# Kernel optimization log

Hardware: AMD Instinct MI355X
Metric: run time of the kernel (lower is better)

The kernel has to match this reference:

```python
import jax, jax.numpy as jnp
import numpy as np

DIM = 512; NHEAD = 8; DHEAD = 64; INNER = NHEAD * DHEAD
CTX = 1024; NOCT = int(np.ceil(np.log2(CTX))) + 1  # 11
B = 8; SEQ = 256; MEM = 768


def positional_encoding(ctx, num_oct):
    # matches Attention.positional_encoding on coords=arange(ctx).view(ctx,1),
    # start_octave = 1 - num_oct
    coords = jnp.arange(ctx, dtype=jnp.float32)[:, None, None]        # (ctx,1,1)
    octaves = jnp.arange(1 - num_oct, 1, dtype=jnp.float32)           # (num_oct,)
    mult = (2.0 ** octaves) * np.pi
    scaled = (coords * mult).reshape(ctx, num_oct)                    # (ctx, num_oct)
    return jnp.concatenate([jnp.sin(scaled), jnp.cos(scaled)], axis=-1)  # (ctx, 2*num_oct)


def get_shifts(mem, seq, ctx):
    coords = jnp.arange(mem + seq - 1, -1, -1) - (seq - 1)            # (mem+seq,)
    shifts = coords[None, :] + jnp.arange(seq)[:, None]               # (seq, mem+seq)
    oob = (shifts < 0) | (shifts > ctx - 1)
    bias = jnp.where(oob, -jnp.inf, 0.0).astype(jnp.float32)
    return jnp.clip(shifts, 0, ctx - 1), bias


def setup_inputs() -> dict:
    key = jax.random.key(0)
    ks = jax.random.split(key, 8)
    s = 0.02
    return {
        "x": jax.random.normal(ks[0], (B, SEQ, DIM), jnp.float32),
        "memory": jax.random.normal(ks[1], (B, MEM, DIM), jnp.float32),
        "W_qkv": jax.random.normal(ks[2], (DIM, 3 * INNER), jnp.float32) * s,
        "W_rel": jax.random.normal(ks[3], (2 * NOCT, INNER), jnp.float32) * s,
        "W_out": jax.random.normal(ks[4], (INNER, DIM), jnp.float32) * s,
        "b_out": jnp.zeros((DIM,), jnp.float32),
        "u_emb": jax.random.normal(ks[5], (DHEAD,), jnp.float32),
        "v_emb": jax.random.normal(ks[6], (DHEAD,), jnp.float32),
    }


def reference(x, memory, W_qkv, W_rel, W_out, b_out, u_emb, v_emb):
    b, seq, _ = x.shape
    mem = memory.shape[1]
    total = mem + seq
    scale = DHEAD ** -0.5

    shifts, bias = get_shifts(mem, seq, CTX)                          # (seq,total) each
    R = positional_encoding(CTX, NOCT)                                # (CTX, 2*NOCT)
    kr = (R @ W_rel)[shifts].reshape(seq, total, NHEAD, DHEAD)        # n m h d

    qkv = jnp.concatenate([memory, x], axis=1) @ W_qkv                # (b,total,3*INNER)
    q, k, v = jnp.split(qkv, 3, axis=-1)

    def heads(t):
        return t.reshape(b, total, NHEAD, DHEAD).transpose(0, 2, 1, 3)  # b h m d

    q = heads(q)[:, :, mem:]                                          # b h n d (queries only over x)
    k = heads(k)
    v = heads(v)

    term_a = jnp.einsum('bhnd,bhmd->bhnm', q, k)
    term_b = jnp.einsum('bhnd,nmhd->bhnm', q, kr)
    term_c = jnp.einsum('d,bhmd->bhm', u_emb, k)[:, :, None, :]        # broadcast over n
    term_d = jnp.einsum('d,nmhd->hnm', v_emb, kr)[None]                # broadcast over b

    dots = (term_a + term_b + term_c + term_d) * scale + bias          # banded -inf mask
    attn = jax.nn.softmax(dots, axis=-1)                               # dropout p=0 -> identity
    out = jnp.einsum('bhnm,bhmd->bnhd', attn, v).reshape(b, seq, INNER)
    return out @ W_out + b_out
```

## Files before the change

### kernel.cpp

```cpp
#include <hip/hip_runtime.h>
#include <hip/hip_bf16.h>
#include <math.h>

typedef unsigned short u16;
typedef unsigned int u32;
typedef __attribute__((ext_vector_type(8))) short short8;
typedef __attribute__((ext_vector_type(4))) float floatx4;

constexpr int kB     = 8;
constexpr int kSEQ   = 256;
constexpr int kMEM   = 768;
constexpr int kTOTAL = 1024;

__device__ __forceinline__ float bf2f(u16 u) {
  return __uint_as_float(((u32)u) << 16);
}
__device__ __forceinline__ u16 f2bf(float f) {
  __hip_bfloat16 h = __float2bfloat16(f);
  return *reinterpret_cast<u16*>(&h);
}
__device__ __forceinline__ void gload_lds16(const u16* g, u16* l) {
  __builtin_amdgcn_global_load_lds(
      (__attribute__((address_space(1))) const unsigned int*)g,
      (__attribute__((address_space(3))) unsigned int*)l, 16, 0, 0);
}

__device__ __forceinline__ void wtconv_body(
    const float* __restrict__ W, u16* __restrict__ Wt, int K, int N,
    int n0, int k0, int tid, float (*tile)[65])
{
  int r = tid >> 4, c4 = (tid & 15) * 4;
#pragma unroll
  for (int v = 0; v < 4; v++) {
    float4 w4 = *(const float4*)(W + (size_t)(k0 + v * 16 + r) * N + n0 + c4);
    tile[v * 16 + r][c4 + 0] = w4.x;
    tile[v * 16 + r][c4 + 1] = w4.y;
    tile[v * 16 + r][c4 + 2] = w4.z;
    tile[v * 16 + r][c4 + 3] = w4.w;
  }
  __syncthreads();
#pragma unroll
  for (int v = 0; v < 4; v++) {
    int rn = v * 16 + r;
    ushort4 o;
    o.x = f2bf(tile[c4 + 0][rn]);
    o.y = f2bf(tile[c4 + 1][rn]);
    o.z = f2bf(tile[c4 + 2][rn]);
    o.w = f2bf(tile[c4 + 3][rn]);
    *(ushort4*)(Wt + (size_t)(n0 + rn) * K + k0 + c4) = o;
  }
}

__global__ __launch_bounds__(256) void prep_kernel(
    const float* __restrict__ x, const float* __restrict__ memf,
    const float* __restrict__ W_qkv, const float* __restrict__ W_out,
    const float* __restrict__ W_rel, const float* __restrict__ v_emb,
    const float* __restrict__ u_emb,
    u16* __restrict__ Xb, u16* __restrict__ WqkvT, u16* __restrict__ WoutT,
    u16* __restrict__ Rrel_bf, float* __restrict__ vR)
{
  __shared__ float tile[64][65];
  __shared__ float pe[22];
  __shared__ float prod[512];
  int bid = blockIdx.x;
  int t = threadIdx.x;
  if (bid < 1024) {
    int s = bid;
    if (t < 22) {
      int o = (t < 11) ? t : (t - 11);
      float mult = ldexpf(3.14159265358979323846f, o - 10);
      float ang = (float)s * mult;
      pe[t] = (t < 11) ? sinf(ang) : cosf(ang);
    }
    __syncthreads();
#pragma unroll
    for (int c = 0; c < 2; c++) {
      int j = t + c * 256;
      float acc = 0.f;
#pragma unroll
      for (int o = 0; o < 22; ++o) acc += pe[o] * W_rel[o * 512 + j];
      u16 rbf = f2bf(acc);
      Rrel_bf[(size_t)s * 512 + j] = rbf;
      prod[j] = acc * v_emb[j & 63] - bf2f(rbf) * u_emb[j & 63];
    }
    __syncthreads();
    if (t < 8) {
      float a = 0.f;
#pragma unroll 8
      for (int d = 0; d < 64; d++) a += prod[t * 64 + d];
      vR[t * 1024 + s] = a * 0.125f;
    }
  } else if (bid < 3072) {
    int idx = (bid - 1024) * 256 + t;
    int row = idx >> 6, c8 = idx & 63;
    int b = row >> 10, pos = row & 1023;
    const float* src = (pos < kMEM)
        ? memf + (size_t)(b * kMEM + pos) * 512
        : x    + (size_t)(b * kSEQ + pos - kMEM) * 512;
    const float4* s4 = (const float4*)(src + c8 * 8);
    float4 a = s4[0], bb = s4[1];
    u16 tmp[8] = {f2bf(a.x),  f2bf(a.y),  f2bf(a.z),  f2bf(a.w),
                  f2bf(bb.x), f2bf(bb.y), f2bf(bb.z), f2bf(bb.w)};
    *(uint4*)(Xb + (size_t)row * 512 + c8 * 8) = *(uint4*)tmp;
  } else if (bid < 3264) {
    int r = bid - 3072;
    wtconv_body(W_qkv, WqkvT, 512, 1536, (r % 24) * 64, (r / 24) * 64, t, tile);
  } else {
    int r = bid - 3264;
    wtconv_body(W_out, WoutT, 512, 512, (r % 8) * 64, (r / 8) * 64, t, tile);
  }
}

__global__ __launch_bounds__(256) void gemm_qkv(
    const u16* __restrict__ A, const u16* __restrict__ Bt,
    u16* __restrict__ Cbf, const float* __restrict__ uq)
{
  __shared__ u16 As[64 * 64];
  __shared__ u16 Bs[128 * 64];
  int tid = threadIdx.x;
  int id = blockIdx.y * gridDim.x + blockIdx.x;
  int bm = (id % 128) * 64, bn = (id / 128) * 128;
  if (bn < 512 && ((bm >> 6) & 15) < 12) return;
  int ln = tid & 15, quad = (tid >> 4) & 3, w = tid >> 6;
  int moff = (w >> 1) * 32, noff = (w & 1) * 64;
  int l7 = ln & 7;
  floatx4 acc[2][4];
#pragma unroll
  for (int mi = 0; mi < 2; mi++)
#pragma unroll
    for (int ni = 0; ni < 4; ni++) acc[mi][ni] = (floatx4){0.f, 0.f, 0.f, 0.f};

  int srow[4], sgch[4];
#pragma unroll
  for (int v = 0; v < 4; v++) {
    int f = v * 256 + tid;
    srow[v] = f >> 3;
    sgch[v] = (f & 7) ^ ((f >> 3) & 7);
  }

  for (int ks = 0; ks < 8; ks++) {
    int k0 = ks * 64;
#pragma unroll
    for (int v = 0; v < 2; v++)
      gload_lds16(A + (size_t)(bm + srow[v]) * 512 + k0 + sgch[v] * 8,
                  &As[(v * 256 + tid) * 8]);
#pragma unroll
    for (int v = 0; v < 4; v++)
      gload_lds16(Bt + (size_t)(bn + srow[v]) * 512 + k0 + sgch[v] * 8,
                  &Bs[(v * 256 + tid) * 8]);
    __syncthreads();
#pragma unroll
    for (int kb = 0; kb < 2; kb++) {
      short8 af[2], bfr[4];
#pragma unroll
      for (int mi = 0; mi < 2; mi++) {
        int row = moff + mi * 16 + ln;
        af[mi] = *(const short8*)&As[row * 64 + (((quad + 4 * kb) ^ l7) << 3)];
      }
#pragma unroll
      for (int ni = 0; ni < 4; ni++) {
        int row = noff + ni * 16 + ln;
        bfr[ni] = *(const short8*)&Bs[row * 64 + (((quad + 4 * kb) ^ l7) << 3)];
      }
#pragma unroll
      for (int mi = 0; mi < 2; mi++)
#pragma unroll
        for (int ni = 0; ni < 4; ni++)
          acc[mi][ni] = __builtin_amdgcn_mfma_f32_16x16x32_bf16(
              af[mi], bfr[ni], acc[mi][ni], 0, 0, 0);
    }
    __syncthreads();
  }

  int r0 = bm + moff + quad * 4;
#pragma unroll
  for (int ni = 0; ni < 4; ni++) {
    int col = bn + noff + ni * 16 + ln;
    bool isq = col < 512;
    float scale = isq ? 0.125f : 1.f;
    float uadd = isq ? uq[col & 63] : 0.f;
#pragma unroll
    for (int mi = 0; mi < 2; mi++) {
#pragma unroll
      for (int r = 0; r < 4; r++) {
        int row = r0 + mi * 16 + r;
        Cbf[(size_t)row * 1536 + col] = f2bf((acc[mi][ni][r] + uadd) * scale);
      }
    }
  }
}

__global__ __launch_bounds__(256) void attn_mfma(
    const u16* __restrict__ qkv_bf, const u16* __restrict__ Rrel_bf,
    const float* __restrict__ vR,
    u16* __restrict__ Opart, float* __restrict__ lbuf)
{
  constexpr int LD = 72;
  __shared__ u16 Vt[2][64 * LD];
  __shared__ u16 Ps[64 * LD];

  int h = blockIdx.x;
  int nt = blockIdx.y >> 2, p = blockIdx.y & 3;
  int b = blockIdx.z;
  int n0 = nt * 64, bh = b * 8 + h;
  int tid = threadIdx.x;
  int w = tid >> 6, lane = tid & 63;
  int l15 = lane & 15, quad = lane >> 4, q8 = quad * 8;

  int sr0 = tid >> 3, sc8 = tid & 7;
  int sr1 = (256 + tid) >> 3;
  int vg0 = ((sr0 >> 3) ^ sc8) * 8 + (sr0 & 7);
  int vg1 = ((sr1 >> 3) ^ sc8) * 8 + (sr1 & 7);

  const u16* kpart = qkv_bf + (size_t)(b * kTOTAL) * 1536 + 512 + h * 64;
  const float* vRh = vR + h * 1024;
  int s_base_w = kMEM + n0 + 16 * w;

  const u16* qrow = qkv_bf + (size_t)(b * kTOTAL + kMEM + n0 + 16 * w + l15) * 1536 + h * 64;
  short8 qf0 = *(const short8*)(qrow + q8);
  short8 qf1 = *(const short8*)(qrow + 32 + q8);

  int bidx[4];
#pragma unroll
  for (int r = 0; r < 4; r++) {
    int il = 4 * quad + r;
    bidx[r] = ((quad << 4) | ((il + 15 - l15) & 15)) << 2;
  }

  auto load_V = [&](int mtu, int mtv, uint4 (&vr)[4]) {
    const u16* va = kpart + (size_t)mtu * 64 * 1536 + 512;
    const u16* vb = kpart + (size_t)mtv * 64 * 1536 + 512;
    vr[0] = *(const uint4*)(va + (size_t)sr0 * 1536 + sc8 * 8);
    vr[1] = *(const uint4*)(va + (size_t)sr1 * 1536 + sc8 * 8);
    vr[2] = *(const uint4*)(vb + (size_t)sr0 * 1536 + sc8 * 8);
    vr[3] = *(const uint4*)(vb + (size_t)sr1 * 1536 + sc8 * 8);
  };
  auto write_V = [&](uint4 (&vr)[4], u16* bu, u16* bv) {
    const u16* c0 = (const u16*)&vr[0];
    const u16* c1 = (const u16*)&vr[1];
    const u16* c2 = (const u16*)&vr[2];
    const u16* c3 = (const u16*)&vr[3];
#pragma unroll
    for (int i = 0; i < 8; i++) {
      bu[(sc8 * 8 + i) * LD + vg0] = c0[i];
      bu[(sc8 * 8 + i) * LD + vg1] = c1[i];
      bv[(sc8 * 8 + i) * LD + vg0] = c2[i];
      bv[(sc8 * 8 + i) * LD + vg1] = c3[i];
    }
  };
  auto load_K = [&](int mt, short8 (&k0)[4], short8 (&k1)[4]) {
#pragma unroll
    for (int ni = 0; ni < 4; ni++) {
      const u16* kr = kpart + (size_t)(mt * 64 + 16 * ni + l15) * 1536;
      k0[ni] = *(const short8*)(kr + q8);
      k1[ni] = *(const short8*)(kr + 32 + q8);
    }
  };
  auto load_R = [&](int sb, short8 (&r0)[5], short8 (&r1)[5], float (&vc)[5]) {
#pragma unroll
    for (int ct = 0; ct < 5; ct++) {
      int s = sb - 63 + 16 * ct + l15;
      s = min(max(s, 0), 1023);
      const u16* rr = Rrel_bf + (size_t)s * 512 + h * 64;
      r0[ct] = *(const short8*)(rr + q8);
      r1[ct] = *(const short8*)(rr + 32 + q8);
      vc[ct] = vRh[s];
    }
  };

  floatx4 o_acc[4];
  float l_i[4];
#pragma unroll
  for (int r = 0; r < 4; r++) l_i[r] = 0.f;
#pragma unroll
  for (int nd = 0; nd < 4; nd++) o_acc[nd] = (floatx4){0.f, 0.f, 0.f, 0.f};

  auto do_T = [&](short8 (&rb0)[5], short8 (&rb1)[5], float (&vRc)[5],
                  float (&tf)[5][4]) {
    __builtin_amdgcn_s_setprio(1);
#pragma unroll
    for (int ct = 0; ct < 5; ct++) {
      floatx4 t = (floatx4){0.f, 0.f, 0.f, 0.f};
      t = __builtin_amdgcn_mfma_f32_16x16x32_bf16(qf0, rb0[ct], t, 0, 0, 0);
      t = __builtin_amdgcn_mfma_f32_16x16x32_bf16(qf1, rb1[ct], t, 0, 0, 0);
#pragma unroll
      for (int r = 0; r < 4; r++) tf[ct][r] = t[r] + vRc[ct];
    }
    __builtin_amdgcn_s_setprio(0);
  };
  auto do_tsh = [&](float (&tf)[5][4], float (&tsh)[4][4]) {
#pragma unroll
    for (int ni = 0; ni < 4; ni++) {
#pragma unroll
      for (int r = 0; r < 4; r++) {
        int il = 4 * quad + r;
        float tv = (l15 < il) ? tf[4 - ni][r] : tf[3 - ni][r];
        tsh[ni][r] = __int_as_float(
            __builtin_amdgcn_ds_bpermute(bidx[r], __float_as_int(tv)));
      }
    }
  };
  auto do_QK = [&](short8 (&kb0)[4], short8 (&kb1)[4], floatx4 (&sa)[4]) {
    __builtin_amdgcn_s_setprio(1);
#pragma unroll
    for (int ni = 0; ni < 4; ni++) {
      floatx4 s4 = (floatx4){0.f, 0.f, 0.f, 0.f};
      s4 = __builtin_amdgcn_mfma_f32_16x16x32_bf16(qf0, kb0[ni], s4, 0, 0, 0);
      s4 = __builtin_amdgcn_mfma_f32_16x16x32_bf16(qf1, kb1[ni], s4, 0, 0, 0);
      sa[ni] = s4;
    }
    __builtin_amdgcn_s_setprio(0);
  };
  auto do_logits = [&](floatx4 (&sa)[4], float (&tsh)[4][4], int sb) {
#pragma unroll
    for (int ni = 0; ni < 4; ni++) {
#pragma unroll
      for (int r = 0; r < 4; r++) {
        int il = 4 * quad + r;
        float val = sa[ni][r] + tsh[ni][r];
        if ((16 * ni + l15) > (sb + il)) val = -1e30f;
        float e = __expf(val);
        l_i[r] += e;
        int prow = 16 * w + il;
        Ps[prow * LD + (l15 & 7) + (((2 * ni + (l15 >> 3)) ^ (prow >> 3)) << 3)] =
            f2bf(e);
      }
    }
  };
  auto do_PV = [&](const u16* VtX) {
    int rowq = 16 * w + l15, rr3q = rowq >> 3;
    short8 pa0 = *(const short8*)&Ps[rowq * LD + ((quad ^ rr3q) << 3)];
    short8 pa1 = *(const short8*)&Ps[rowq * LD + (((quad + 4) ^ rr3q) << 3)];
    __builtin_amdgcn_s_setprio(1);
#pragma unroll
    for (int nd = 0; nd < 4; nd++) {
      int rowv = 16 * nd + l15, rr3v = rowv >> 3;
      short8 vb0 = *(const short8*)&VtX[rowv * LD + ((quad ^ rr3v) << 3)];
      short8 vb1 = *(const short8*)&VtX[rowv * LD + (((quad + 4) ^ rr3v) << 3)];
      o_acc[nd] = __builtin_amdgcn_mfma_f32_16x16x32_bf16(pa0, vb0, o_acc[nd], 0, 0, 0);
      o_acc[nd] = __builtin_amdgcn_mfma_f32_16x16x32_bf16(pa1, vb1, o_acc[nd], 0, 0, 0);
    }
    __builtin_amdgcn_s_setprio(0);
  };

  short8 rbU0[5], rbU1[5];
  float vRcU[5];
  uint4 vsl[4];
  {
    uint4 v0[4];
    load_V(p, p + 4, v0);
    write_V(v0, Vt[0], Vt[1]);
  }
  load_V(p + 8, p + 12, vsl);
  load_R(s_base_w - 64 * p, rbU0, rbU1, vRcU);
  __syncthreads();

#pragma unroll
  for (int g = 0; g < 2; g++) {
    int mtU = p + 8 * g, mtV = mtU + 4;
    int sbU = s_base_w - 64 * mtU, sbV = s_base_w - 64 * mtV;

    if (g == 1) write_V(vsl, Vt[0], Vt[1]);

    short8 kbU0[4], kbU1[4];
    load_K(mtU, kbU0, kbU1);

    float tfU[5][4], tshU[4][4];
    do_T(rbU0, rbU1, vRcU, tfU);
    do_tsh(tfU, tshU);

    short8 rbV0[5], rbV1[5];
    float vRcV[5];
    load_R(sbV, rbV0, rbV1, vRcV);

    floatx4 saU[4];
    do_QK(kbU0, kbU1, saU);
    do_logits(saU, tshU, sbU);

    short8 kbV0[4], kbV1[4];
    load_K(mtV, kbV0, kbV1);
    if (g == 0)
      load_R(s_base_w - 64 * (p + 8), rbU0, rbU1, vRcU);

    float tfV[5][4], tshV[4][4];
    do_T(rbV0, rbV1, vRcV, tfV);
    do_tsh(tfV, tshV);

    if (g == 1) __syncthreads();
    do_PV(Vt[0]);

    floatx4 saV[4];
    do_QK(kbV0, kbV1, saV);
    do_logits(saV, tshV, sbV);
    do_PV(Vt[1]);

    if (g == 0) __syncthreads();
  }

  int pbase = (p * 64 + bh) * 256;
#pragma unroll
  for (int r = 0; r < 4; r++) {
    float l = l_i[r];
#pragma unroll
    for (int off = 1; off < 16; off <<= 1)
      l += __shfl_xor(l, off, 64);
    int n = n0 + 16 * w + 4 * quad + r;
    u16* orow = Opart + ((size_t)(pbase + n) << 6) + l15;
#pragma unroll
    for (int nd = 0; nd < 4; nd++)
      orow[16 * nd] = f2bf(o_acc[nd][r]);
    if (l15 == 0) lbuf[pbase + n] = l;
  }
}

__global__ __launch_bounds__(256) void gemm_out_fused(
    const u16* __restrict__ Opart, const float* __restrict__ lbuf,
    const u16* __restrict__ Bt, float* __restrict__ Cf,
    const float* __restrict__ bias)
{
  __shared__ u16 As[64 * 64];
  __shared__ u16 Bs[64 * 64];
  __shared__ float invl[64][8];
  int tid = threadIdx.x;
  int id = blockIdx.y * gridDim.x + blockIdx.x;
  int bm = (id % 32) * 64, bn = (id / 32) * 64;
  int ln = tid & 15, quad = (tid >> 4) & 3, w = tid >> 6;
  int moff = (w >> 1) * 32, noff = (w & 1) * 32;
  int l7 = ln & 7;

#pragma unroll
  for (int e = tid; e < 512; e += 256) {
    int r = e >> 3, hh = e & 7;
    int grow = bm + r, b = grow >> 8, n = grow & 255;
    int bh = b * 8 + hh;
    float den = 0.f;
#pragma unroll
    for (int p = 0; p < 4; p++) den += lbuf[((p * 64 + bh) << 8) + n];
    invl[r][hh] = 1.f / den;
  }

  floatx4 acc[2][2];
#pragma unroll
  for (int mi = 0; mi < 2; mi++)
#pragma unroll
    for (int ni = 0; ni < 2; ni++) acc[mi][ni] = (floatx4){0.f, 0.f, 0.f, 0.f};

  int srow[2], sgch[2];
#pragma unroll
  for (int v = 0; v < 2; v++) {
    int f = v * 256 + tid;
    srow[v] = f >> 3;
    sgch[v] = (f & 7) ^ ((f >> 3) & 7);
  }

  int sr = tid >> 2, dq = (tid & 3) * 16;
  int growq = bm + sr, bq = growq >> 8, nq = growq & 255;
  int cg0 = dq >> 3;
  u16* dst0 = &As[sr * 64 + ((cg0 ^ (sr & 7)) << 3)];
  u16* dst1 = &As[sr * 64 + (((cg0 + 1) ^ (sr & 7)) << 3)];

  __syncthreads();

  for (int ks = 0; ks < 8; ks++) {
    int k0 = ks * 64;
#pragma unroll
    for (int v = 0; v < 2; v++)
      gload_lds16(Bt + (size_t)(bn + srow[v]) * 512 + k0 + sgch[v] * 8,
                  &Bs[(v * 256 + tid) * 8]);

    {
      const u16* ob = Opart + (((size_t)(bq * 8 + ks) << 8) + nq) * 64 + dq;
      float inv = invl[sr][ks];
      float sum[16];
#pragma unroll
      for (int j = 0; j < 16; j++) sum[j] = 0.f;
#pragma unroll
      for (int p = 0; p < 4; p++) {
        const u16* src = ob + ((size_t)p << 20);
        uint4 r0 = *(const uint4*)src;
        uint4 r1 = *(const uint4*)(src + 8);
        const u16* u0 = (const u16*)&r0;
        const u16* u1 = (const u16*)&r1;
#pragma unroll
        for (int j = 0; j < 8; j++) sum[j] += bf2f(u0[j]);
#pragma unroll
        for (int j = 0; j < 8; j++) sum[8 + j] += bf2f(u1[j]);
      }
      u16 ov[16];
#pragma unroll
      for (int j = 0; j < 16; j++) ov[j] = f2bf(sum[j] * inv);
      *(uint4*)dst0 = *(uint4*)&ov[0];
      *(uint4*)dst1 = *(uint4*)&ov[8];
    }
    __syncthreads();
#pragma unroll
    for (int kb = 0; kb < 2; kb++) {
      short8 af[2], bfr[2];
#pragma unroll
      for (int mi = 0; mi < 2; mi++) {
        int row = moff + mi * 16 + ln;
        af[mi] = *(const short8*)&As[row * 64 + (((quad + 4 * kb) ^ l7) << 3)];
      }
#pragma unroll
      for (int ni = 0; ni < 2; ni++) {
        int row = noff + ni * 16 + ln;
        bfr[ni] = *(const short8*)&Bs[row * 64 + (((quad + 4 * kb) ^ l7) << 3)];
      }
#pragma unroll
      for (int mi = 0; mi < 2; mi++)
#pragma unroll
        for (int ni = 0; ni < 2; ni++)
          acc[mi][ni] = __builtin_amdgcn_mfma_f32_16x16x32_bf16(
              af[mi], bfr[ni], acc[mi][ni], 0, 0, 0);
    }
    __syncthreads();
  }

  int r0 = bm + moff + quad * 4;
#pragma unroll
  for (int ni = 0; ni < 2; ni++) {
    int col = bn + noff + ni * 16 + ln;
    float cv = bias[col];
#pragma unroll
    for (int mi = 0; mi < 2; mi++) {
#pragma unroll
      for (int r = 0; r < 4; r++) {
        int row = r0 + mi * 16 + r;
        Cf[(size_t)row * 512 + col] = acc[mi][ni][r] + cv;
      }
    }
  }
}

extern "C" void kernel_launch(void* const* d_in, const int* in_sizes, int n_in,
                              void* d_out, int out_size, void* d_ws, size_t ws_size,
                              hipStream_t stream) {
  (void)in_sizes; (void)n_in; (void)out_size; (void)ws_size;
  const float* x      = (const float*)d_in[0];
  const float* memory = (const float*)d_in[1];
  const float* W_qkv  = (const float*)d_in[2];
  const float* W_rel  = (const float*)d_in[3];
  const float* W_out  = (const float*)d_in[4];
  const float* b_out  = (const float*)d_in[5];
  const float* u_emb  = (const float*)d_in[6];
  const float* v_emb  = (const float*)d_in[7];
  float* out = (float*)d_out;

  char* ws = (char*)d_ws;
  u16*   qkv_bf  = (u16*)ws;                         ws += (size_t)12582912 * 2;
  u16*   Xcat_bf = (u16*)ws;                         ws += (size_t)4194304 * 2;
  u16*   Opart   = (u16*)ws;                         ws += (size_t)4194304 * 2;
  float* lbuf    = (float*)ws;                       ws += (size_t)65536 * 4;
  u16*   WqkvT   = (u16*)ws;                         ws += (size_t)786432 * 2;
  u16*   WoutT   = (u16*)ws;                         ws += (size_t)262144 * 2;
  u16*   Rrel_bf = (u16*)ws;                         ws += (size_t)524288 * 2;
  float* vR      = (float*)ws;                       ws += (size_t)8192 * 4;

  prep_kernel<<<3328, 256, 0, stream>>>(
      x, memory, W_qkv, W_out, W_rel, v_emb, u_emb,
      Xcat_bf, WqkvT, WoutT, Rrel_bf, vR);

  gemm_qkv<<<dim3(12, 128), 256, 0, stream>>>(
      Xcat_bf, WqkvT, qkv_bf, u_emb);

  attn_mfma<<<dim3(8, 16, 8), 256, 0, stream>>>(
      qkv_bf, Rrel_bf, vR, Opart, lbuf);

  gemm_out_fused<<<dim3(8, 32), 256, 0, stream>>>(
      Opart, lbuf, WoutT, out, b_out);
}
```

Baseline: 157.4 us.

## Prefetch O partials and narrow output GEMM tiles; drop setprio in attention

The output GEMM now uses 64x32 tiles, which doubles the grid to 512 blocks. It also register-double-buffers the next k-step's Opart partial loads so that global latency overlaps the reduction and MFMA work. Separately, the s_setprio bracketing around the MFMA sections in the attention kernel is removed. The gemm changes aim at better occupancy and latency hiding, at the cost of more register pressure and twice the A-tile reduction work overall (each A tile is now recomputed for two N halves).

```diff
diff --git a/kernel.cpp b/kernel.cpp
--- a/kernel.cpp
+++ b/kernel.cpp
@@ -277,7 +277,6 @@
 
   auto do_T = [&](short8 (&rb0)[5], short8 (&rb1)[5], float (&vRc)[5],
                   float (&tf)[5][4]) {
-    __builtin_amdgcn_s_setprio(1);
 #pragma unroll
     for (int ct = 0; ct < 5; ct++) {
       floatx4 t = (floatx4){0.f, 0.f, 0.f, 0.f};
@@ -286,7 +285,6 @@
 #pragma unroll
       for (int r = 0; r < 4; r++) tf[ct][r] = t[r] + vRc[ct];
     }
-    __builtin_amdgcn_s_setprio(0);
   };
   auto do_tsh = [&](float (&tf)[5][4], float (&tsh)[4][4]) {
 #pragma unroll
@@ -301,7 +299,6 @@
     }
   };
   auto do_QK = [&](short8 (&kb0)[4], short8 (&kb1)[4], floatx4 (&sa)[4]) {
-    __builtin_amdgcn_s_setprio(1);
 #pragma unroll
     for (int ni = 0; ni < 4; ni++) {
       floatx4 s4 = (floatx4){0.f, 0.f, 0.f, 0.f};
@@ -309,7 +306,6 @@
       s4 = __builtin_amdgcn_mfma_f32_16x16x32_bf16(qf1, kb1[ni], s4, 0, 0, 0);
       sa[ni] = s4;
     }
-    __builtin_amdgcn_s_setprio(0);
   };
   auto do_logits = [&](floatx4 (&sa)[4], float (&tsh)[4][4], int sb) {
 #pragma unroll
@@ -331,7 +327,6 @@
     int rowq = 16 * w + l15, rr3q = rowq >> 3;
     short8 pa0 = *(const short8*)&Ps[rowq * LD + ((quad ^ rr3q) << 3)];
     short8 pa1 = *(const short8*)&Ps[rowq * LD + (((quad + 4) ^ rr3q) << 3)];
-    __builtin_amdgcn_s_setprio(1);
 #pragma unroll
     for (int nd = 0; nd < 4; nd++) {
       int rowv = 16 * nd + l15, rr3v = rowv >> 3;
@@ -340,7 +335,6 @@
       o_acc[nd] = __builtin_amdgcn_mfma_f32_16x16x32_bf16(pa0, vb0, o_acc[nd], 0, 0, 0);
       o_acc[nd] = __builtin_amdgcn_mfma_f32_16x16x32_bf16(pa1, vb1, o_acc[nd], 0, 0, 0);
     }
-    __builtin_amdgcn_s_setprio(0);
   };
 
   short8 rbU0[5], rbU1[5];
@@ -419,14 +413,35 @@
     const float* __restrict__ bias)
 {
   __shared__ u16 As[64 * 64];
-  __shared__ u16 Bs[64 * 64];
+  __shared__ u16 Bs[32 * 64];
   __shared__ float invl[64][8];
   int tid = threadIdx.x;
   int id = blockIdx.y * gridDim.x + blockIdx.x;
-  int bm = (id % 32) * 64, bn = (id / 32) * 64;
+  int bm = (id % 32) * 64, bn = (id / 32) * 32;
   int ln = tid & 15, quad = (tid >> 4) & 3, w = tid >> 6;
-  int moff = (w >> 1) * 32, noff = (w & 1) * 32;
   int l7 = ln & 7;
+
+  int sr = tid >> 2, dq = (tid & 3) * 16;
+  int growq = bm + sr, bq = growq >> 8, nq = growq & 255;
+  int cg0 = dq >> 3;
+  u16* dst0 = &As[sr * 64 + ((cg0 ^ (sr & 7)) << 3)];
+  u16* dst1 = &As[sr * 64 + (((cg0 + 1) ^ (sr & 7)) << 3)];
+
+  auto load_O = [&](int ks, uint4 (&pf)[8]) {
+    const u16* ob = Opart + (((size_t)(bq * 8 + ks) << 8) + nq) * 64 + dq;
+#pragma unroll
+    for (int p = 0; p < 4; p++) {
+      const u16* src = ob + ((size_t)p << 20);
+      pf[2 * p]     = *(const uint4*)src;
+      pf[2 * p + 1] = *(const uint4*)(src + 8);
+    }
+  };
+
+  int srowB = tid >> 3;
+  int sgchB = (tid & 7) ^ ((tid >> 3) & 7);
+
+  uint4 pfA[8], pfB[8];
+  load_O(0, pfA);
 
 #pragma unroll
   for (int e = tid; e < 512; e += 256) {
@@ -439,48 +454,26 @@
     invl[r][hh] = 1.f / den;
   }
 
-  floatx4 acc[2][2];
-#pragma unroll
-  for (int mi = 0; mi < 2; mi++)
-#pragma unroll
-    for (int ni = 0; ni < 2; ni++) acc[mi][ni] = (floatx4){0.f, 0.f, 0.f, 0.f};
-
-  int srow[2], sgch[2];
-#pragma unroll
-  for (int v = 0; v < 2; v++) {
-    int f = v * 256 + tid;
-    srow[v] = f >> 3;
-    sgch[v] = (f & 7) ^ ((f >> 3) & 7);
-  }
-
-  int sr = tid >> 2, dq = (tid & 3) * 16;
-  int growq = bm + sr, bq = growq >> 8, nq = growq & 255;
-  int cg0 = dq >> 3;
-  u16* dst0 = &As[sr * 64 + ((cg0 ^ (sr & 7)) << 3)];
-  u16* dst1 = &As[sr * 64 + (((cg0 + 1) ^ (sr & 7)) << 3)];
+  floatx4 acc[2];
+#pragma unroll
+  for (int ni = 0; ni < 2; ni++) acc[ni] = (floatx4){0.f, 0.f, 0.f, 0.f};
 
   __syncthreads();
 
-  for (int ks = 0; ks < 8; ks++) {
-    int k0 = ks * 64;
-#pragma unroll
-    for (int v = 0; v < 2; v++)
-      gload_lds16(Bt + (size_t)(bn + srow[v]) * 512 + k0 + sgch[v] * 8,
-                  &Bs[(v * 256 + tid) * 8]);
+  auto body = [&](int ks, uint4 (&cur)[8], uint4 (&nxt)[8], bool last) {
+    gload_lds16(Bt + (size_t)(bn + srowB) * 512 + ks * 64 + sgchB * 8,
+                &Bs[tid * 8]);
+    if (!last) load_O(ks + 1, nxt);
 
     {
-      const u16* ob = Opart + (((size_t)(bq * 8 + ks) << 8) + nq) * 64 + dq;
       float inv = invl[sr][ks];
       float sum[16];
 #pragma unroll
       for (int j = 0; j < 16; j++) sum[j] = 0.f;
 #pragma unroll
       for (int p = 0; p < 4; p++) {
-        const u16* src = ob + ((size_t)p << 20);
-        uint4 r0 = *(const uint4*)src;
-        uint4 r1 = *(const uint4*)(src + 8);
-        const u16* u0 = (const u16*)&r0;
-        const u16* u1 = (const u16*)&r1;
+        const u16* u0 = (const u16*)&cur[2 * p];
+        const u16* u1 = (const u16*)&cur[2 * p + 1];
 #pragma unroll
         for (int j = 0; j < 8; j++) sum[j] += bf2f(u0[j]);
 #pragma unroll
@@ -493,42 +486,41 @@
       *(uint4*)dst1 = *(uint4*)&ov[8];
     }
     __syncthreads();
+
 #pragma unroll
     for (int kb = 0; kb < 2; kb++) {
-      short8 af[2], bfr[2];
-#pragma unroll
-      for (int mi = 0; mi < 2; mi++) {
-        int row = moff + mi * 16 + ln;
-        af[mi] = *(const short8*)&As[row * 64 + (((quad + 4 * kb) ^ l7) << 3)];
-      }
+      int rowA = w * 16 + ln;
+      short8 af = *(const short8*)&As[rowA * 64 + (((quad + 4 * kb) ^ l7) << 3)];
+      short8 bfr[2];
 #pragma unroll
       for (int ni = 0; ni < 2; ni++) {
-        int row = noff + ni * 16 + ln;
+        int row = ni * 16 + ln;
         bfr[ni] = *(const short8*)&Bs[row * 64 + (((quad + 4 * kb) ^ l7) << 3)];
       }
 #pragma unroll
-      for (int mi = 0; mi < 2; mi++)
-#pragma unroll
-        for (int ni = 0; ni < 2; ni++)
-          acc[mi][ni] = __builtin_amdgcn_mfma_f32_16x16x32_bf16(
-              af[mi], bfr[ni], acc[mi][ni], 0, 0, 0);
+      for (int ni = 0; ni < 2; ni++)
+        acc[ni] = __builtin_amdgcn_mfma_f32_16x16x32_bf16(af, bfr[ni], acc[ni], 0, 0, 0);
     }
     __syncthreads();
-  }
-
-  int r0 = bm + moff + quad * 4;
+  };
+
+  body(0, pfA, pfB, false);
+  body(1, pfB, pfA, false);
+  body(2, pfA, pfB, false);
+  body(3, pfB, pfA, false);
+  body(4, pfA, pfB, false);
+  body(5, pfB, pfA, false);
+  body(6, pfA, pfB, false);
+  body(7, pfB, pfA, true);
+
+  int r0 = bm + w * 16 + quad * 4;
 #pragma unroll
   for (int ni = 0; ni < 2; ni++) {
-    int col = bn + noff + ni * 16 + ln;
+    int col = bn + ni * 16 + ln;
     float cv = bias[col];
 #pragma unroll
-    for (int mi = 0; mi < 2; mi++) {
-#pragma unroll
-      for (int r = 0; r < 4; r++) {
-        int row = r0 + mi * 16 + r;
-        Cf[(size_t)row * 512 + col] = acc[mi][ni][r] + cv;
-      }
-    }
+    for (int r = 0; r < 4; r++)
+      Cf[(size_t)(r0 + r) * 512 + col] = acc[ni][r] + cv;
   }
 }
 
@@ -566,6 +558,6 @@
   attn_mfma<<<dim3(8, 16, 8), 256, 0, stream>>>(
       qkv_bf, Rrel_bf, vR, Opart, lbuf);
 
-  gemm_out_fused<<<dim3(8, 32), 256, 0, stream>>>(
+  gemm_out_fused<<<dim3(16, 32), 256, 0, stream>>>(
       Opart, lbuf, WoutT, out, b_out);
 }
```

After: 152.4 us. 3.1% less time.
